# Performance work log

Measured on AMD Instinct MI355X. Metric: run time of the kernel, lower is better.

Reference implementation:

```python
import jax, jax.numpy as jnp
import numpy as np

N_NODES = 50000
N_EDGES = 1600000
DIM_IN = 128
DIM_OUT = 128
EPS = 1e-10


def setup_inputs() -> dict:
    key = jax.random.key(0)
    k1, k2, k3, k4, k5 = jax.random.split(key, 5)
    feat_in = jax.random.normal(k1, (N_NODES, DIM_IN), dtype=jnp.float32)
    rows = jax.random.randint(k2, (N_EDGES,), 0, N_NODES, dtype=jnp.int32)
    cols = jax.random.randint(k3, (N_EDGES,), 0, N_NODES, dtype=jnp.int32)
    # normalized adjacency values (positive, ~1/deg scale)
    vals = jax.random.uniform(k4, (N_EDGES,), dtype=jnp.float32) / 32.0
    W = jax.random.normal(k5, (DIM_OUT, DIM_IN), dtype=jnp.float32) * 0.05
    b = jnp.zeros((DIM_OUT,), dtype=jnp.float32)
    scale = jnp.ones((DIM_OUT,), dtype=jnp.float32)
    offset = jnp.zeros((DIM_OUT,), dtype=jnp.float32)
    return {"feat_in": feat_in, "rows": rows, "cols": cols, "vals": vals,
            "W": W, "b": b, "scale": scale, "offset": offset}


def reference(feat_in, rows, cols, vals, W, b, scale, offset):
    # torch.sparse.mm(adj_norm, feat_in): gather source features, scale by
    # edge value, scatter-add into destination rows.
    msgs = vals[:, None] * feat_in[cols]                       # [E, D_in]
    feat_aggr = jax.ops.segment_sum(msgs, rows, num_segments=N_NODES)  # [N, D_in]
    # f_lin (nn.Linear): x @ W.T + b
    feat_trans = feat_aggr @ W.T + b                           # [N, D_out]
    # act = ReLU
    a = jax.nn.relu(feat_trans)
    # f_norm: per-row (feature-dim) normalization, biased variance
    mean = jnp.mean(a, axis=1, keepdims=True)
    var = jnp.mean((a - mean) ** 2, axis=1, keepdims=True) + EPS
    feat_out = (a - mean) * scale * jax.lax.rsqrt(var) + offset
    return feat_out
```

## Files before the change

kernel.cpp:

```cpp
#include <hip/hip_runtime.h>

typedef unsigned int uint;

#define N_NODES 50000
#define N_EDGES 1600000
#define DIM 128
#define LN_EPS 1e-10f

#define ROWS_PER_BUCKET 64
#define N_BUCKETS 782
#define BUCKET_CAP 2560
#define EPB 8192
#define SB 196
#define FCB 1563
#define GPAD 16
#define CAPR 76

__device__ __forceinline__ uint f2bf(float x) {
    uint u = __float_as_uint(x);
    return (u + 0x7FFFu + ((u >> 16) & 1u)) >> 16;
}

__global__ __launch_bounds__(1024) void prep(
    const float* __restrict__ feat, const float* __restrict__ W,
    const int* __restrict__ rows, const int* __restrict__ cols,
    const float* __restrict__ vals, int* __restrict__ gcnt,
    int2* __restrict__ perm, uint* __restrict__ featb_u,
    uint* __restrict__ wpk_u)
{
    __shared__ int  cnt[N_BUCKETS];
    __shared__ int  gbase[N_BUCKETS];
    __shared__ int  lbase[N_BUCKETS];
    __shared__ int  lcur[N_BUCKETS];
    __shared__ int  csum[64];
    __shared__ int2 stageE[EPB];
    const int bx = blockIdx.x;
    const int t  = threadIdx.x;

    if (bx >= SB) {
        int cb = bx - SB;
        if (cb < FCB) {
            int i = cb * 1024 + t;
            if (i < N_NODES * DIM / 4) {
                float4 v = ((const float4*)feat)[i];
                ((uint2*)featb_u)[i] = make_uint2(
                    f2bf(v.x) | (f2bf(v.y) << 16),
                    f2bf(v.z) | (f2bf(v.w) << 16));
            }
        } else {
            for (int idx = t; idx < 8192; idx += 1024) {
                int g = idx >> 8, rem = idx & 255;
                int l = rem >> 2, k = rem & 3, i = 4 * g + k;
                wpk_u[idx] = f2bf(W[l * DIM + i]) |
                             (f2bf(W[(l + 64) * DIM + i]) << 16);
            }
        }
        return;
    }

    for (int i = t; i < N_BUCKETS; i += 1024) cnt[i] = 0;
    __syncthreads();
    const int base = bx * EPB;
    for (int k = 0; k < EPB; k += 1024) {
        int e = base + k + t;
        if (e < N_EDGES) atomicAdd(&cnt[rows[e] >> 6], 1);
    }
    __syncthreads();

    for (int i = t; i < N_BUCKETS; i += 1024) {
        int c = cnt[i];
        gbase[i] = c ? atomicAdd(&gcnt[i * GPAD], c) : 0;
    }
    if (t < 64) {
        int s = 0;
        for (int j = 0; j < 13; ++j) {
            int idx = t * 13 + j;
            if (idx < N_BUCKETS) s += cnt[idx];
        }
        csum[t] = s;
    }
    __syncthreads();
    if (t == 0) {
        int s = 0;
        for (int i = 0; i < 64; ++i) { int c = csum[i]; csum[i] = s; s += c; }
    }
    __syncthreads();
    if (t < 64) {
        int run = csum[t];
        for (int j = 0; j < 13; ++j) {
            int idx = t * 13 + j;
            if (idx < N_BUCKETS) { lbase[idx] = run; lcur[idx] = run; run += cnt[idx]; }
        }
    }
    __syncthreads();

    for (int k = 0; k < EPB; k += 1024) {
        int e = base + k + t;
        if (e < N_EDGES) {
            int r = rows[e];
            int b = r >> 6;
            int pos = atomicAdd(&lcur[b], 1);
            stageE[pos] = make_int2(
                (uint)cols[e] | ((uint)(r & 63) << 16) | ((uint)b << 22),
                __float_as_int(vals[e]));
        }
    }
    __syncthreads();

    int total = lbase[N_BUCKETS - 1] + cnt[N_BUCKETS - 1];
    for (int k = 0; k < EPB; k += 1024) {
        int j = k + t;
        if (j < total) {
            int2 p = stageE[j];
            uint b = ((uint)p.x) >> 22;
            int pos = gbase[b] + (j - lbase[b]);
            if (pos < BUCKET_CAP)
                perm[(size_t)b * BUCKET_CAP + pos] = p;
        }
    }
}

__global__ __launch_bounds__(512, 8) void agg_fused(
    const int2* __restrict__ perm, const int* __restrict__ gcnt,
    const unsigned short* __restrict__ featb, const uint4* __restrict__ wpk,
    const float* __restrict__ bias, const float* __restrict__ scale,
    const float* __restrict__ offset, float* __restrict__ out)
{
    __shared__ int2 lists[32 * CAPR];
    __shared__ int  lcnt[32];

    const int t = threadIdx.x;
    float* rowsbuf = (float*)lists;

    const int b  = blockIdx.x >> 1;
    const int lo = (blockIdx.x & 1) * 32;
    if (t < 32) lcnt[t] = 0;
    __syncthreads();

    int n = gcnt[b * GPAD];
    if (n > BUCKET_CAP) n = BUCKET_CAP;
    const int2* pb = perm + (size_t)b * BUCKET_CAP;

    for (int e = t; e < n; e += 512) {
        int2 p = pb[e];
        int rl = ((p.x >> 16) & 63) - lo;
        if ((uint)rl < 32u) {
            int pos = atomicAdd(&lcnt[rl], 1);
            if (pos < CAPR)
                lists[rl * CAPR + pos] = make_int2(p.x & 0xFFFF, p.y);
        }
    }
    __syncthreads();

    const int lane = t & 63;
    const int wid  = t >> 6;
    const int rb   = wid * 4;

    float ax[4], ay[4];
    #pragma unroll
    for (int j = 0; j < 4; ++j) {
        int rl = rb + j;
        int cnt = lcnt[rl];
        if (cnt > CAPR) cnt = CAPR;
        const int2* L = &lists[rl * CAPR];
        float sx = 0.f, sy = 0.f;
        int e = 0;
        for (; e + 7 < cnt; e += 8) {
            int2 p[8]; uint g[8];
            #pragma unroll
            for (int k = 0; k < 8; ++k) p[k] = L[e + k];
            #pragma unroll
            for (int k = 0; k < 8; ++k)
                g[k] = ((const uint*)(featb + (size_t)p[k].x * DIM))[lane];
            #pragma unroll
            for (int k = 0; k < 8; ++k) {
                float v = __int_as_float(p[k].y);
                sx = fmaf(v, __uint_as_float(g[k] << 16), sx);
                sy = fmaf(v, __uint_as_float(g[k] & 0xFFFF0000u), sy);
            }
        }
        for (; e < cnt; ++e) {
            int2 p = L[e];
            uint g = ((const uint*)(featb + (size_t)p.x * DIM))[lane];
            float v = __int_as_float(p.y);
            sx = fmaf(v, __uint_as_float(g << 16), sx);
            sy = fmaf(v, __uint_as_float(g & 0xFFFF0000u), sy);
        }
        ax[j] = sx; ay[j] = sy;
    }
    __syncthreads();

    #pragma unroll
    for (int j = 0; j < 4; ++j)
        ((float2*)rowsbuf)[(rb + j) * 64 + lane] = make_float2(ax[j], ay[j]);
    __syncthreads();

    const float bb0 = bias[lane],   bb1 = bias[lane + 64];
    const float sc0 = scale[lane],  sc1 = scale[lane + 64];
    const float of0 = offset[lane], of1 = offset[lane + 64];

    const float4* R0 = (const float4*)(rowsbuf + (rb + 0) * DIM);
    const float4* R1 = (const float4*)(rowsbuf + (rb + 1) * DIM);
    const float4* R2 = (const float4*)(rowsbuf + (rb + 2) * DIM);
    const float4* R3 = (const float4*)(rowsbuf + (rb + 3) * DIM);

    float x0 = bb0, y0 = bb1, x1 = bb0, y1 = bb1;
    float x2 = bb0, y2 = bb1, x3 = bb0, y3 = bb1;

    #pragma unroll 4
    for (int g = 0; g < 32; ++g) {
        uint4 wv = wpk[g * 64 + lane];
        float4 a0 = R0[g], a1 = R1[g], a2 = R2[g], a3 = R3[g];
        float w0, w1;
        w0 = __uint_as_float(wv.x << 16); w1 = __uint_as_float(wv.x & 0xFFFF0000u);
        x0 = fmaf(a0.x, w0, x0);  y0 = fmaf(a0.x, w1, y0);
        x1 = fmaf(a1.x, w0, x1);  y1 = fmaf(a1.x, w1, y1);
        x2 = fmaf(a2.x, w0, x2);  y2 = fmaf(a2.x, w1, y2);
        x3 = fmaf(a3.x, w0, x3);  y3 = fmaf(a3.x, w1, y3);
        w0 = __uint_as_float(wv.y << 16); w1 = __uint_as_float(wv.y & 0xFFFF0000u);
        x0 = fmaf(a0.y, w0, x0);  y0 = fmaf(a0.y, w1, y0);
        x1 = fmaf(a1.y, w0, x1);  y1 = fmaf(a1.y, w1, y1);
        x2 = fmaf(a2.y, w0, x2);  y2 = fmaf(a2.y, w1, y2);
        x3 = fmaf(a3.y, w0, x3);  y3 = fmaf(a3.y, w1, y3);
        w0 = __uint_as_float(wv.z << 16); w1 = __uint_as_float(wv.z & 0xFFFF0000u);
        x0 = fmaf(a0.z, w0, x0);  y0 = fmaf(a0.z, w1, y0);
        x1 = fmaf(a1.z, w0, x1);  y1 = fmaf(a1.z, w1, y1);
        x2 = fmaf(a2.z, w0, x2);  y2 = fmaf(a2.z, w1, y2);
        x3 = fmaf(a3.z, w0, x3);  y3 = fmaf(a3.z, w1, y3);
        w0 = __uint_as_float(wv.w << 16); w1 = __uint_as_float(wv.w & 0xFFFF0000u);
        x0 = fmaf(a0.w, w0, x0);  y0 = fmaf(a0.w, w1, y0);
        x1 = fmaf(a1.w, w0, x1);  y1 = fmaf(a1.w, w1, y1);
        x2 = fmaf(a2.w, w0, x2);  y2 = fmaf(a2.w, w1, y2);
        x3 = fmaf(a3.w, w0, x3);  y3 = fmaf(a3.w, w1, y3);
    }

    #pragma unroll
    for (int j = 0; j < 4; ++j) {
        int r = b * ROWS_PER_BUCKET + lo + rb + j;
        if (r >= N_NODES) continue;
        float A0 = (j == 0) ? x0 : (j == 1) ? x1 : (j == 2) ? x2 : x3;
        float A1 = (j == 0) ? y0 : (j == 1) ? y1 : (j == 2) ? y2 : y3;
        A0 = fmaxf(A0, 0.0f);
        A1 = fmaxf(A1, 0.0f);

        float s = A0 + A1;
        #pragma unroll
        for (int off = 32; off >= 1; off >>= 1) s += __shfl_xor(s, off, 64);
        float mean = s * (1.0f / 128.0f);

        float d0 = A0 - mean, d1 = A1 - mean;
        float q = d0 * d0 + d1 * d1;
        #pragma unroll
        for (int off = 32; off >= 1; off >>= 1) q += __shfl_xor(q, off, 64);
        float rstd = rsqrtf(q * (1.0f / 128.0f) + LN_EPS);

        size_t rowp = (size_t)r * DIM;
        out[rowp + lane]      = d0 * sc0 * rstd + of0;
        out[rowp + lane + 64] = d1 * sc1 * rstd + of1;
    }
}

extern "C" void kernel_launch(void* const* d_in, const int* in_sizes, int n_in,
                              void* d_out, int out_size, void* d_ws, size_t ws_size,
                              hipStream_t stream) {
    const float* feat_in = (const float*)d_in[0];
    const int*   rows    = (const int*)d_in[1];
    const int*   cols    = (const int*)d_in[2];
    const float* vals    = (const float*)d_in[3];
    const float* W       = (const float*)d_in[4];
    const float* bias    = (const float*)d_in[5];
    const float* scale   = (const float*)d_in[6];
    const float* offset  = (const float*)d_in[7];
    float* out = (float*)d_out;

    char* p = (char*)d_ws;
    int2* perm = (int2*)p;                 p += (size_t)N_BUCKETS * BUCKET_CAP * 8;
    unsigned short* featb = (unsigned short*)p;
                                           p += (size_t)N_NODES * DIM * 2;
    uint* wpk = (uint*)p;                  p += 32768;
    int*  gcnt = (int*)p;                  p += (size_t)N_BUCKETS * GPAD * 4;

    hipMemsetAsync(gcnt, 0, (size_t)N_BUCKETS * GPAD * sizeof(int), stream);

    prep<<<SB + FCB + 1, 1024, 0, stream>>>(feat_in, W, rows, cols, vals,
                                            gcnt, perm, (uint*)featb, wpk);
    agg_fused<<<N_BUCKETS * 2, 512, 0, stream>>>(perm, gcnt, featb,
                                                 (const uint4*)wpk,
                                                 bias, scale, offset, out);
}
```

Measured before the change: 193.1 us.

## Bucket edges by 32-row groups and split prep into convert and scatter kernels

Edges are now bucketed per 32-row group instead of per 64-row bucket. Each aggregation block therefore reads only its own edges and no longer filters out half of a shared bucket, which halves the perm reads per block. The bf16 conversion and W packing move to a separate kernel, and the scatter kernel stashes rows in shared memory to avoid reading them twice. This adds a kernel launch, needs more shared memory per scatter block, and uses a tighter per-group capacity that could overflow on skewed inputs.

```diff
diff --git a/kernel.cpp b/kernel.cpp
--- a/kernel.cpp
+++ b/kernel.cpp
@@ -7,12 +7,11 @@
 #define DIM 128
 #define LN_EPS 1e-10f
 
-#define ROWS_PER_BUCKET 64
-#define N_BUCKETS 782
-#define BUCKET_CAP 2560
+#define ROWS_PER_GROUP 32
+#define N_GROUPS 1563
+#define GROUP_CAP 1344
 #define EPB 8192
 #define SB 196
-#define FCB 1563
 #define GPAD 16
 #define CAPR 76
 
@@ -21,101 +20,106 @@
     return (u + 0x7FFFu + ((u >> 16) & 1u)) >> 16;
 }
 
-__global__ __launch_bounds__(1024) void prep(
+__global__ __launch_bounds__(256) void convert_pack(
     const float* __restrict__ feat, const float* __restrict__ W,
+    uint* __restrict__ featb_u, uint* __restrict__ wpk_u)
+{
+    const int b = blockIdx.x;
+    const int t = threadIdx.x;
+    if (b < 3125) {
+        int i = b * 512 + t;
+        float4 v0 = ((const float4*)feat)[i];
+        float4 v1 = ((const float4*)feat)[i + 256];
+        ((uint2*)featb_u)[i] = make_uint2(
+            f2bf(v0.x) | (f2bf(v0.y) << 16), f2bf(v0.z) | (f2bf(v0.w) << 16));
+        ((uint2*)featb_u)[i + 256] = make_uint2(
+            f2bf(v1.x) | (f2bf(v1.y) << 16), f2bf(v1.z) | (f2bf(v1.w) << 16));
+    } else {
+        for (int idx = t; idx < 8192; idx += 256) {
+            int g = idx >> 8, rem = idx & 255;
+            int l = rem >> 2, k = rem & 3, i = 4 * g + k;
+            wpk_u[idx] = f2bf(W[l * DIM + i]) |
+                         (f2bf(W[(l + 64) * DIM + i]) << 16);
+        }
+    }
+}
+
+__global__ __launch_bounds__(1024) void scatter(
     const int* __restrict__ rows, const int* __restrict__ cols,
     const float* __restrict__ vals, int* __restrict__ gcnt,
-    int2* __restrict__ perm, uint* __restrict__ featb_u,
-    uint* __restrict__ wpk_u)
+    int2* __restrict__ perm)
 {
-    __shared__ int  cnt[N_BUCKETS];
-    __shared__ int  gbase[N_BUCKETS];
-    __shared__ int  lbase[N_BUCKETS];
-    __shared__ int  lcur[N_BUCKETS];
-    __shared__ int  csum[64];
+    __shared__ int  cnt[N_GROUPS];
+    __shared__ int  gbase[N_GROUPS];
+    __shared__ int  lcur[N_GROUPS];
+    __shared__ int  csum[128];
+    __shared__ int  stash[EPB];
     __shared__ int2 stageE[EPB];
     const int bx = blockIdx.x;
     const int t  = threadIdx.x;
 
-    if (bx >= SB) {
-        int cb = bx - SB;
-        if (cb < FCB) {
-            int i = cb * 1024 + t;
-            if (i < N_NODES * DIM / 4) {
-                float4 v = ((const float4*)feat)[i];
-                ((uint2*)featb_u)[i] = make_uint2(
-                    f2bf(v.x) | (f2bf(v.y) << 16),
-                    f2bf(v.z) | (f2bf(v.w) << 16));
-            }
-        } else {
-            for (int idx = t; idx < 8192; idx += 1024) {
-                int g = idx >> 8, rem = idx & 255;
-                int l = rem >> 2, k = rem & 3, i = 4 * g + k;
-                wpk_u[idx] = f2bf(W[l * DIM + i]) |
-                             (f2bf(W[(l + 64) * DIM + i]) << 16);
-            }
-        }
-        return;
-    }
-
-    for (int i = t; i < N_BUCKETS; i += 1024) cnt[i] = 0;
-    __syncthreads();
+    for (int i = t; i < N_GROUPS; i += 1024) cnt[i] = 0;
+    __syncthreads();
+
     const int base = bx * EPB;
     for (int k = 0; k < EPB; k += 1024) {
         int e = base + k + t;
-        if (e < N_EDGES) atomicAdd(&cnt[rows[e] >> 6], 1);
-    }
-    __syncthreads();
-
-    for (int i = t; i < N_BUCKETS; i += 1024) {
+        int r = (e < N_EDGES) ? rows[e] : -1;
+        stash[k + t] = r;
+        if (r >= 0) atomicAdd(&cnt[r >> 5], 1);
+    }
+    __syncthreads();
+
+    for (int i = t; i < N_GROUPS; i += 1024) {
         int c = cnt[i];
         gbase[i] = c ? atomicAdd(&gcnt[i * GPAD], c) : 0;
     }
-    if (t < 64) {
+    if (t < 128) {
         int s = 0;
         for (int j = 0; j < 13; ++j) {
             int idx = t * 13 + j;
-            if (idx < N_BUCKETS) s += cnt[idx];
+            if (idx < N_GROUPS) s += cnt[idx];
         }
         csum[t] = s;
     }
     __syncthreads();
     if (t == 0) {
         int s = 0;
-        for (int i = 0; i < 64; ++i) { int c = csum[i]; csum[i] = s; s += c; }
-    }
-    __syncthreads();
-    if (t < 64) {
+        for (int i = 0; i < 128; ++i) { int c = csum[i]; csum[i] = s; s += c; }
+    }
+    __syncthreads();
+    if (t < 128) {
         int run = csum[t];
         for (int j = 0; j < 13; ++j) {
             int idx = t * 13 + j;
-            if (idx < N_BUCKETS) { lbase[idx] = run; lcur[idx] = run; run += cnt[idx]; }
+            if (idx < N_GROUPS) { lcur[idx] = run; run += cnt[idx]; }
         }
     }
     __syncthreads();
 
     for (int k = 0; k < EPB; k += 1024) {
         int e = base + k + t;
-        if (e < N_EDGES) {
-            int r = rows[e];
-            int b = r >> 6;
-            int pos = atomicAdd(&lcur[b], 1);
+        int r = stash[k + t];
+        if (r >= 0) {
+            int g = r >> 5;
+            int pos = atomicAdd(&lcur[g], 1);
             stageE[pos] = make_int2(
-                (uint)cols[e] | ((uint)(r & 63) << 16) | ((uint)b << 22),
+                (uint)cols[e] | ((uint)(r & 31) << 16) | ((uint)g << 21),
                 __float_as_int(vals[e]));
         }
     }
     __syncthreads();
 
-    int total = lbase[N_BUCKETS - 1] + cnt[N_BUCKETS - 1];
+    int total = lcur[N_GROUPS - 1];
     for (int k = 0; k < EPB; k += 1024) {
         int j = k + t;
         if (j < total) {
             int2 p = stageE[j];
-            uint b = ((uint)p.x) >> 22;
-            int pos = gbase[b] + (j - lbase[b]);
-            if (pos < BUCKET_CAP)
-                perm[(size_t)b * BUCKET_CAP + pos] = p;
+            uint g = ((uint)p.x) >> 21;
+            int lb = lcur[g] - cnt[g];
+            int pos = gbase[g] + (j - lb);
+            if (pos < GROUP_CAP)
+                perm[(size_t)g * GROUP_CAP + pos] = p;
         }
     }
 }
@@ -132,23 +136,20 @@
     const int t = threadIdx.x;
     float* rowsbuf = (float*)lists;
 
-    const int b  = blockIdx.x >> 1;
-    const int lo = (blockIdx.x & 1) * 32;
+    const int b = blockIdx.x;
     if (t < 32) lcnt[t] = 0;
     __syncthreads();
 
     int n = gcnt[b * GPAD];
-    if (n > BUCKET_CAP) n = BUCKET_CAP;
-    const int2* pb = perm + (size_t)b * BUCKET_CAP;
+    if (n > GROUP_CAP) n = GROUP_CAP;
+    const int2* pb = perm + (size_t)b * GROUP_CAP;
 
     for (int e = t; e < n; e += 512) {
         int2 p = pb[e];
-        int rl = ((p.x >> 16) & 63) - lo;
-        if ((uint)rl < 32u) {
-            int pos = atomicAdd(&lcnt[rl], 1);
-            if (pos < CAPR)
-                lists[rl * CAPR + pos] = make_int2(p.x & 0xFFFF, p.y);
-        }
+        int rl = (p.x >> 16) & 31;
+        int pos = atomicAdd(&lcnt[rl], 1);
+        if (pos < CAPR)
+            lists[rl * CAPR + pos] = make_int2(p.x & 0xFFFF, p.y);
     }
     __syncthreads();
 
@@ -236,7 +237,7 @@
 
     #pragma unroll
     for (int j = 0; j < 4; ++j) {
-        int r = b * ROWS_PER_BUCKET + lo + rb + j;
+        int r = b * ROWS_PER_GROUP + rb + j;
         if (r >= N_NODES) continue;
         float A0 = (j == 0) ? x0 : (j == 1) ? x1 : (j == 2) ? x2 : x3;
         float A1 = (j == 0) ? y0 : (j == 1) ? y1 : (j == 2) ? y2 : y3;
@@ -274,17 +275,17 @@
     float* out = (float*)d_out;
 
     char* p = (char*)d_ws;
-    int2* perm = (int2*)p;                 p += (size_t)N_BUCKETS * BUCKET_CAP * 8;
+    int2* perm = (int2*)p;                 p += (size_t)N_GROUPS * GROUP_CAP * 8;
     unsigned short* featb = (unsigned short*)p;
                                            p += (size_t)N_NODES * DIM * 2;
     uint* wpk = (uint*)p;                  p += 32768;
-    int*  gcnt = (int*)p;                  p += (size_t)N_BUCKETS * GPAD * 4;
-
-    hipMemsetAsync(gcnt, 0, (size_t)N_BUCKETS * GPAD * sizeof(int), stream);
-
-    prep<<<SB + FCB + 1, 1024, 0, stream>>>(feat_in, W, rows, cols, vals,
-                                            gcnt, perm, (uint*)featb, wpk);
-    agg_fused<<<N_BUCKETS * 2, 512, 0, stream>>>(perm, gcnt, featb,
-                                                 (const uint4*)wpk,
-                                                 bias, scale, offset, out);
-}
+    int*  gcnt = (int*)p;                  p += (size_t)N_GROUPS * GPAD * 4;
+
+    hipMemsetAsync(gcnt, 0, (size_t)N_GROUPS * GPAD * sizeof(int), stream);
+
+    convert_pack<<<3126, 256, 0, stream>>>(feat_in, W, (uint*)featb, wpk);
+    scatter<<<SB, 1024, 0, stream>>>(rows, cols, vals, gcnt, perm);
+    agg_fused<<<N_GROUPS, 512, 0, stream>>>(perm, gcnt, featb,
+                                            (const uint4*)wpk,
+                                            bias, scale, offset, out);
+}
```

Result: slower. 209.8 us (+8.7%).

## Use bf16 MFMA for the fused linear layer instead of scalar FMAs

Applied to the files above, without the earlier changes.

Replaces the per-lane scalar FMA matrix multiply of aggregated rows by W with bf16 MFMA 16x16x32 instructions. Aggregated rows are packed to bf16 in padded shared memory, W is stored as plain row-major bf16, and results pass through a padded fp32 shared buffer for the ReLU and layer norm. It also drops the lbase shared array in prep and relaxes launch bounds from 8 to 6 blocks per CU. This adds bf16 rounding of the aggregated activations and extra syncs in exchange for fewer ALU instructions.

```diff
diff --git a/kernel.cpp b/kernel.cpp
--- a/kernel.cpp
+++ b/kernel.cpp
@@ -1,6 +1,9 @@
 #include <hip/hip_runtime.h>
 
 typedef unsigned int uint;
+typedef unsigned short ushort;
+typedef __attribute__((ext_vector_type(8))) short short8;
+typedef __attribute__((ext_vector_type(4))) float floatx4;
 
 #define N_NODES 50000
 #define N_EDGES 1600000
@@ -26,11 +29,10 @@
     const int* __restrict__ rows, const int* __restrict__ cols,
     const float* __restrict__ vals, int* __restrict__ gcnt,
     int2* __restrict__ perm, uint* __restrict__ featb_u,
-    uint* __restrict__ wpk_u)
+    ushort* __restrict__ wbf)
 {
     __shared__ int  cnt[N_BUCKETS];
     __shared__ int  gbase[N_BUCKETS];
-    __shared__ int  lbase[N_BUCKETS];
     __shared__ int  lcur[N_BUCKETS];
     __shared__ int  csum[64];
     __shared__ int2 stageE[EPB];
@@ -48,12 +50,8 @@
                     f2bf(v.z) | (f2bf(v.w) << 16));
             }
         } else {
-            for (int idx = t; idx < 8192; idx += 1024) {
-                int g = idx >> 8, rem = idx & 255;
-                int l = rem >> 2, k = rem & 3, i = 4 * g + k;
-                wpk_u[idx] = f2bf(W[l * DIM + i]) |
-                             (f2bf(W[(l + 64) * DIM + i]) << 16);
-            }
+            for (int idx = t; idx < DIM * DIM; idx += 1024)
+                wbf[idx] = (ushort)f2bf(W[idx]);
         }
         return;
     }
@@ -89,7 +87,7 @@
         int run = csum[t];
         for (int j = 0; j < 13; ++j) {
             int idx = t * 13 + j;
-            if (idx < N_BUCKETS) { lbase[idx] = run; lcur[idx] = run; run += cnt[idx]; }
+            if (idx < N_BUCKETS) { lcur[idx] = run; run += cnt[idx]; }
         }
     }
     __syncthreads();
@@ -107,31 +105,32 @@
     }
     __syncthreads();
 
-    int total = lbase[N_BUCKETS - 1] + cnt[N_BUCKETS - 1];
+    int total = lcur[N_BUCKETS - 1];
     for (int k = 0; k < EPB; k += 1024) {
         int j = k + t;
         if (j < total) {
             int2 p = stageE[j];
             uint b = ((uint)p.x) >> 22;
-            int pos = gbase[b] + (j - lbase[b]);
+            int lb = lcur[b] - cnt[b];
+            int pos = gbase[b] + (j - lb);
             if (pos < BUCKET_CAP)
                 perm[(size_t)b * BUCKET_CAP + pos] = p;
         }
     }
 }
 
-__global__ __launch_bounds__(512, 8) void agg_fused(
+__global__ __launch_bounds__(512, 6) void agg_fused(
     const int2* __restrict__ perm, const int* __restrict__ gcnt,
-    const unsigned short* __restrict__ featb, const uint4* __restrict__ wpk,
+    const ushort* __restrict__ featb, const ushort* __restrict__ wbf,
     const float* __restrict__ bias, const float* __restrict__ scale,
     const float* __restrict__ offset, float* __restrict__ out)
 {
     __shared__ int2 lists[32 * CAPR];
+    ushort* rowsbuf = (ushort*)lists;
+    float*  Cbuf    = (float*)lists;
     __shared__ int  lcnt[32];
 
     const int t = threadIdx.x;
-    float* rowsbuf = (float*)lists;
-
     const int b  = blockIdx.x >> 1;
     const int lo = (blockIdx.x & 1) * 32;
     if (t < 32) lcnt[t] = 0;
@@ -191,57 +190,48 @@
     __syncthreads();
 
     #pragma unroll
-    for (int j = 0; j < 4; ++j)
-        ((float2*)rowsbuf)[(rb + j) * 64 + lane] = make_float2(ax[j], ay[j]);
-    __syncthreads();
-
-    const float bb0 = bias[lane],   bb1 = bias[lane + 64];
+    for (int j = 0; j < 4; ++j) {
+        uint pk = f2bf(ax[j]) | (f2bf(ay[j]) << 16);
+        *(uint*)&rowsbuf[(rb + j) * 136 + 2 * lane] = pk;
+    }
+    __syncthreads();
+
+    const int l15  = lane & 15;
+    const int quad = lane >> 4;
+    const int n0   = wid * 16 + l15;
+    const float bb = bias[n0];
+
+    floatx4 acc0 = {0.f, 0.f, 0.f, 0.f};
+    floatx4 acc1 = {0.f, 0.f, 0.f, 0.f};
+    #pragma unroll
+    for (int kt = 0; kt < 4; ++kt) {
+        int k0 = kt * 32 + quad * 8;
+        short8 af0 = *(const short8*)&rowsbuf[l15 * 136 + k0];
+        short8 af1 = *(const short8*)&rowsbuf[(l15 + 16) * 136 + k0];
+        short8 bf  = *(const short8*)&wbf[n0 * DIM + k0];
+        acc0 = __builtin_amdgcn_mfma_f32_16x16x32_bf16(af0, bf, acc0, 0, 0, 0);
+        acc1 = __builtin_amdgcn_mfma_f32_16x16x32_bf16(af1, bf, acc1, 0, 0, 0);
+    }
+    __syncthreads();
+
+    #pragma unroll
+    for (int r = 0; r < 4; ++r) {
+        int m = quad * 4 + r;
+        Cbuf[m * 132 + n0]        = acc0[r] + bb;
+        Cbuf[(m + 16) * 132 + n0] = acc1[r] + bb;
+    }
+    __syncthreads();
+
     const float sc0 = scale[lane],  sc1 = scale[lane + 64];
     const float of0 = offset[lane], of1 = offset[lane + 64];
 
-    const float4* R0 = (const float4*)(rowsbuf + (rb + 0) * DIM);
-    const float4* R1 = (const float4*)(rowsbuf + (rb + 1) * DIM);
-    const float4* R2 = (const float4*)(rowsbuf + (rb + 2) * DIM);
-    const float4* R3 = (const float4*)(rowsbuf + (rb + 3) * DIM);
-
-    float x0 = bb0, y0 = bb1, x1 = bb0, y1 = bb1;
-    float x2 = bb0, y2 = bb1, x3 = bb0, y3 = bb1;
-
-    #pragma unroll 4
-    for (int g = 0; g < 32; ++g) {
-        uint4 wv = wpk[g * 64 + lane];
-        float4 a0 = R0[g], a1 = R1[g], a2 = R2[g], a3 = R3[g];
-        float w0, w1;
-        w0 = __uint_as_float(wv.x << 16); w1 = __uint_as_float(wv.x & 0xFFFF0000u);
-        x0 = fmaf(a0.x, w0, x0);  y0 = fmaf(a0.x, w1, y0);
-        x1 = fmaf(a1.x, w0, x1);  y1 = fmaf(a1.x, w1, y1);
-        x2 = fmaf(a2.x, w0, x2);  y2 = fmaf(a2.x, w1, y2);
-        x3 = fmaf(a3.x, w0, x3);  y3 = fmaf(a3.x, w1, y3);
-        w0 = __uint_as_float(wv.y << 16); w1 = __uint_as_float(wv.y & 0xFFFF0000u);
-        x0 = fmaf(a0.y, w0, x0);  y0 = fmaf(a0.y, w1, y0);
-        x1 = fmaf(a1.y, w0, x1);  y1 = fmaf(a1.y, w1, y1);
-        x2 = fmaf(a2.y, w0, x2);  y2 = fmaf(a2.y, w1, y2);
-        x3 = fmaf(a3.y, w0, x3);  y3 = fmaf(a3.y, w1, y3);
-        w0 = __uint_as_float(wv.z << 16); w1 = __uint_as_float(wv.z & 0xFFFF0000u);
-        x0 = fmaf(a0.z, w0, x0);  y0 = fmaf(a0.z, w1, y0);
-        x1 = fmaf(a1.z, w0, x1);  y1 = fmaf(a1.z, w1, y1);
-        x2 = fmaf(a2.z, w0, x2);  y2 = fmaf(a2.z, w1, y2);
-        x3 = fmaf(a3.z, w0, x3);  y3 = fmaf(a3.z, w1, y3);
-        w0 = __uint_as_float(wv.w << 16); w1 = __uint_as_float(wv.w & 0xFFFF0000u);
-        x0 = fmaf(a0.w, w0, x0);  y0 = fmaf(a0.w, w1, y0);
-        x1 = fmaf(a1.w, w0, x1);  y1 = fmaf(a1.w, w1, y1);
-        x2 = fmaf(a2.w, w0, x2);  y2 = fmaf(a2.w, w1, y2);
-        x3 = fmaf(a3.w, w0, x3);  y3 = fmaf(a3.w, w1, y3);
-    }
-
     #pragma unroll
     for (int j = 0; j < 4; ++j) {
-        int r = b * ROWS_PER_BUCKET + lo + rb + j;
+        int rl = rb + j;
+        int r  = b * ROWS_PER_BUCKET + lo + rl;
         if (r >= N_NODES) continue;
-        float A0 = (j == 0) ? x0 : (j == 1) ? x1 : (j == 2) ? x2 : x3;
-        float A1 = (j == 0) ? y0 : (j == 1) ? y1 : (j == 2) ? y2 : y3;
-        A0 = fmaxf(A0, 0.0f);
-        A1 = fmaxf(A1, 0.0f);
+        float A0 = fmaxf(Cbuf[rl * 132 + lane],      0.0f);
+        float A1 = fmaxf(Cbuf[rl * 132 + lane + 64], 0.0f);
 
         float s = A0 + A1;
         #pragma unroll
@@ -275,16 +265,14 @@
 
     char* p = (char*)d_ws;
     int2* perm = (int2*)p;                 p += (size_t)N_BUCKETS * BUCKET_CAP * 8;
-    unsigned short* featb = (unsigned short*)p;
-                                           p += (size_t)N_NODES * DIM * 2;
-    uint* wpk = (uint*)p;                  p += 32768;
+    ushort* featb = (ushort*)p;            p += (size_t)N_NODES * DIM * 2;
+    ushort* wbf = (ushort*)p;              p += DIM * DIM * 2;
     int*  gcnt = (int*)p;                  p += (size_t)N_BUCKETS * GPAD * 4;
 
     hipMemsetAsync(gcnt, 0, (size_t)N_BUCKETS * GPAD * sizeof(int), stream);
 
     prep<<<SB + FCB + 1, 1024, 0, stream>>>(feat_in, W, rows, cols, vals,
-                                            gcnt, perm, (uint*)featb, wpk);
-    agg_fused<<<N_BUCKETS * 2, 512, 0, stream>>>(perm, gcnt, featb,
-                                                 (const uint4*)wpk,
+                                            gcnt, perm, (uint*)featb, wbf);
+    agg_fused<<<N_BUCKETS * 2, 512, 0, stream>>>(perm, gcnt, featb, wbf,
                                                  bias, scale, offset, out);
 }
```

After: 181.4 us. 1.06x faster.
